# Performance work log

Hardware: AMD Instinct MI355X
Metric: run time of the kernel (lower is better)

The kernel has to match this reference:

```python
import jax, jax.numpy as jnp
import numpy as np

V = 32000
MASK_ID = 31999
EPS = 1e-3          # log-linear schedule eps
DT = 0.05           # reverse-step size
NUCLEUS_P = 0.9
NEG_INF = -1000000.0
B, S = 2, 1024


def move_chance(t):
    # BD3-LM log-linear schedule: move_chance(t) = (1 - eps) * t
    return (1.0 - EPS) * t


def nucleus_filter(probs, p):
    # descending sort over vocab
    order = jnp.argsort(-probs, axis=-1)                     # [B,S,V]
    sorted_probs = jnp.take_along_axis(probs, order, axis=-1)
    cum = jnp.cumsum(sorted_probs, axis=-1)
    keep = cum <= p
    keep = keep.at[..., 0].set(True)                          # always keep top-1
    kept = sorted_probs * keep
    inv = jnp.argsort(order, axis=-1)                         # inverse permutation
    filtered = jnp.take_along_axis(kept, inv, axis=-1)        # scatter back
    return filtered / jnp.sum(filtered, axis=-1, keepdims=True)


def setup_inputs() -> dict:
    key = jax.random.key(0)
    k1, k2, k3, k4 = jax.random.split(key, 4)
    x = jax.random.randint(k1, (B, S), 0, V, dtype=jnp.int32)
    m = jax.random.uniform(k4, (B, S)) < 0.5
    x = jnp.where(m, MASK_ID, x)
    logits = jax.random.normal(k2, (B, S, V), dtype=jnp.float32)
    t = jnp.ones((1,), dtype=jnp.float32)
    u = jax.random.uniform(k3, (B, S, V), dtype=jnp.float32)
    return {"x": x, "logits": logits, "t": t, "u": u}


def reference(x, logits, t, u):
    mct = move_chance(t)[..., None]          # [1,1]
    mcs = move_chance(t - DT)[..., None]     # [1,1]
    mask_prob = mcs / mct                    # [1,1], broadcasts over [S,V]

    logits = logits.at[:, :, MASK_ID].set(NEG_INF)
    p_x0 = jax.nn.softmax(logits, axis=-1)   # [B,S,V]
    p_x0 = nucleus_filter(p_x0, NUCLEUS_P)

    q_xs = p_x0 * (1.0 - mask_prob)
    q_xs = q_xs.at[:, :, MASK_ID].set(jnp.squeeze(mask_prob, -1))

    gumbel = -jnp.log(-jnp.log(u + 1e-10) + 1e-10)
    x_new = jnp.argmax(q_xs / (gumbel + 1e-10), axis=-1).astype(x.dtype)

    is_masked = x == MASK_ID
    x_new = jnp.where(is_masked, x_new, x)
    return x_new, p_x0
```

## Files before the change

kernel.cpp:

```cpp
#include <hip/hip_runtime.h>

#define NVOC 32000
#define NV4  (NVOC / 4)
#define MASKID 31999
#define NBINS 1024
#define NTHR 1024
#define LISTCAP 2048

typedef unsigned int u32;
typedef unsigned long long u64;

__device__ __forceinline__ int bin_e(float e) {
    int v = (int)(__float_as_uint(e) >> 17) - 6976;
    v = v < 0 ? 0 : v;
    return v > (NBINS - 1) ? (NBINS - 1) : v;
}

__device__ __forceinline__ u32 fix32(float e) {
    float x = e * 4294967296.0f;
    x = fminf(x, 4294967040.0f);
    return (u32)x;
}

__device__ __forceinline__ u64 shfl_down_u64(u64 v, int off) {
    u32 lo = (u32)(v & 0xFFFFFFFFULL);
    u32 hi = (u32)(v >> 32);
    lo = __shfl_down(lo, off, 64);
    hi = __shfl_down(hi, off, 64);
    return (((u64)hi) << 32) | lo;
}

__global__ __launch_bounds__(NTHR, 8) void mdlm_kernel(
    const int* __restrict__ xin,
    const float* __restrict__ logits,
    const float* __restrict__ tin,
    const float* __restrict__ uin,
    float* __restrict__ out,
    int rows)
{
    __shared__ u64 sHist[NBINS];
    __shared__ u32 sList[LISTCAP];
    __shared__ double sRedD[16];
    __shared__ float sRedF[16];
    __shared__ int sRedI[16];
    __shared__ u64 sRedU[16];
    __shared__ float sZmax, sTT;
    __shared__ int sCnt, sB, sCross, sMaxDrop;
    __shared__ u32 sTau;
    __shared__ u64 sZ, sAs, sSfp;

    const int row = blockIdx.x;
    if (row >= rows) return;
    const int tid = threadIdx.x;
    const float4* lrow4 = (const float4*)(logits + (size_t)row * NVOC);
    const float* urow = uin + (size_t)row * NVOC;
    float* prow = out + (size_t)rows + (size_t)row * NVOC;

    sHist[tid] = 0ULL;
    if (tid == 0) {
        sCnt = 0; sB = -1; sCross = 0; sMaxDrop = -1; sTau = 0xFFFFFFFFu;
        sZ = 0ULL; sSfp = 0ULL; sAs = 0ULL;
        sTT = tin[0];
    }
    __syncthreads();

    float lmax = -3.0e38f;
    for (int v4 = tid; v4 < NV4; v4 += NTHR) {
        float4 f = lrow4[v4];
        if (v4 == (MASKID >> 2)) f.w = -1000000.0f;
        lmax = fmaxf(lmax, fmaxf(fmaxf(f.x, f.y), fmaxf(f.z, f.w)));
    }
    for (int off = 32; off > 0; off >>= 1)
        lmax = fmaxf(lmax, __shfl_down(lmax, off, 64));
    if ((tid & 63) == 0) sRedF[tid >> 6] = lmax;
    __syncthreads();
    if (tid == 0) {
        float m = sRedF[0];
        for (int w = 1; w < NTHR / 64; ++w) m = fmaxf(m, sRedF[w]);
        sZmax = m;
    }
    __syncthreads();
    const float zmax = sZmax;

    u64 zloc = 0ULL;
    for (int v4 = tid; v4 < NV4; v4 += NTHR) {
        float4 f = lrow4[v4];
        if (v4 == (MASKID >> 2)) f.w = -1000000.0f;
        float zz[4] = {f.x, f.y, f.z, f.w};
#pragma unroll
        for (int e4 = 0; e4 < 4; ++e4) {
            float e = __expf(zz[e4] - zmax);
            u32 m = fix32(e);
            atomicAdd(&sHist[bin_e(e)], (u64)m);
            zloc += m;
        }
    }
    for (int off = 32; off > 0; off >>= 1) zloc += shfl_down_u64(zloc, off);
    if ((tid & 63) == 0) sRedU[tid >> 6] = zloc;
    __syncthreads();
    if (tid == 0) {
        u64 z = 0ULL;
        for (int w = 0; w < NTHR / 64; ++w) z += sRedU[w];
        sZ = z;
    }
    __syncthreads();
    const double T = 0.9 * (double)sZ;

    for (int dlt = 1; dlt < NBINS; dlt <<= 1) {
        u64 vv = (tid + dlt < NBINS) ? sHist[tid + dlt] : 0ULL;
        __syncthreads();
        sHist[tid] += vv;
        __syncthreads();
    }
    {
        u64 Ai = sHist[tid];
        u64 As = (tid + 1 < NBINS) ? sHist[tid + 1] : 0ULL;
        bool dropped = ((double)As >= T);
        bool keptf = ((double)Ai <= T);
        if (dropped) atomicMax(&sMaxDrop, tid);
        if (!dropped && !keptf) { sB = tid; sCross = 1; }
    }
    __syncthreads();
    if (tid == 0) {
        int B = sCross ? sB : sMaxDrop;
        sB = B;
        u64 As;
        if (B < 0) As = sHist[0];
        else As = (B + 1 < NBINS) ? sHist[B + 1] : 0ULL;
        sAs = As;
        if (!sCross) sSfp = As;
    }
    __syncthreads();

    const int Bst = sB;
    const int cross = sCross;

    if (cross) {
        for (int v4 = tid; v4 < NV4; v4 += NTHR) {
            float4 f = lrow4[v4];
            if (v4 == (MASKID >> 2)) f.w = -1000000.0f;
            float zz[4] = {f.x, f.y, f.z, f.w};
#pragma unroll
            for (int e4 = 0; e4 < 4; ++e4) {
                float e = __expf(zz[e4] - zmax);
                if (bin_e(e) == Bst) {
                    u32 m = fix32(e);
                    int pos = atomicAdd(&sCnt, 1);
                    if (pos < LISTCAP) sList[pos] = m;
                }
            }
        }
        __syncthreads();
        const int K = sCnt < LISTCAP ? sCnt : LISTCAP;
        for (int jj = tid; jj < K; jj += NTHR) {
            u32 mj = sList[jj];
            u64 s = sAs;
            for (int q2 = 0; q2 < K; ++q2) {
                u32 mv = sList[q2];
                if (mv >= mj) s += (u64)mv;
            }
            if ((double)s <= T) atomicMin(&sTau, mj);
        }
        __syncthreads();
        if (tid == 0) sSfp = sAs;
        __syncthreads();
        u32 tl = sTau;
        if (tl != 0xFFFFFFFFu) {
            u64 part = 0ULL;
            for (int q2 = tid; q2 < K; q2 += NTHR) {
                u32 mv = sList[q2];
                if (mv >= tl) part += (u64)mv;
            }
            if (part) atomicAdd(&sSfp, part);
        }
        __syncthreads();
    }

    u32 tauU;
    {
        u32 tv = sTau;
        u32 edgefix = 0u;
        if (Bst >= 0) edgefix = fix32(__uint_as_float((u32)(Bst + 1 + 6976) << 17));
        if (cross) tauU = (tv != 0xFFFFFFFFu) ? tv : edgefix;
        else       tauU = (Bst < 0) ? 0u : edgefix;
    }

    const double invSd = 4294967296.0 / (double)sSfp;
    const float invSf = (float)invSd;

    const double td = (double)sTT;
    const double mpd = ((1.0 - 1e-3) * (td - 0.05)) / ((1.0 - 1e-3) * td);
    const double omd = 1.0 - mpd;
    const float mpf = (float)mpd;
    const float omf = (float)omd;

    float r1 = -3.0e38f, r2 = -3.0e38f;
    int   i1 = 0,        i2 = 0;
    float e1 = 0.0f,     e2 = 0.0f;
    float u1 = 0.0f,     u2 = 0.0f;
    for (int v4 = tid; v4 < NV4; v4 += NTHR) {
        float4 uf = ((const float4*)urow)[v4];
        float4 f = lrow4[v4];
        if (v4 == (MASKID >> 2)) f.w = -1000000.0f;
        float uu[4] = {uf.x, uf.y, uf.z, uf.w};
        float zz[4] = {f.x, f.y, f.z, f.w};
        float pp[4];
        const int i0 = v4 * 4;
#pragma unroll
        for (int e4 = 0; e4 < 4; ++e4) {
            const int i = i0 + e4;
            float e = __expf(zz[e4] - zmax);
            bool kept = (fix32(e) >= tauU);
            float p = kept ? e * invSf : 0.0f;
            pp[e4] = p;
            float q = p * omf;
            float ug = uu[e4] + 1e-10f;
            float l1 = __logf(ug);
            float w = 1e-10f - l1;
            float g = -__logf(w);
            float r = q * __builtin_amdgcn_rcpf(g + 1e-10f);
            if (r > r1) {
                r2 = r1; i2 = i1; e2 = e1; u2 = u1;
                r1 = r;  i1 = i;  e1 = e;  u1 = uu[e4];
            } else if (r > r2) {
                r2 = r;  i2 = i;  e2 = e;  u2 = uu[e4];
            }
        }
        float4 po;
        po.x = pp[0]; po.y = pp[1]; po.z = pp[2]; po.w = pp[3];
        ((float4*)prow)[v4] = po;
    }
    if (tid == ((MASKID >> 2) & (NTHR - 1))) {
        float um = urow[MASKID];
        float ug = um + 1e-10f;
        float l1 = __logf(ug);
        float w = 1e-10f - l1;
        float g = -__logf(w);
        float rm = mpf * __builtin_amdgcn_rcpf(g + 1e-10f);
        if (rm > r1) {
            r2 = r1; i2 = i1; e2 = e1; u2 = u1;
            r1 = rm; i1 = MASKID; e1 = 0.0f; u1 = um;
        } else if (rm > r2) {
            r2 = rm; i2 = MASKID; e2 = 0.0f; u2 = um;
        }
    }

    double best; int bidx;
    {
        double q;
        if (i1 == MASKID) q = mpd;
        else {
            bool k = (fix32(e1) >= tauU);
            q = k ? (double)e1 * invSd * omd : 0.0;
        }
        double g = -log(-log((double)u1 + 1e-10) + 1e-10);
        best = q / (g + 1e-10);
        bidx = i1;
    }
    {
        double q;
        if (i2 == MASKID) q = mpd;
        else {
            bool k = (fix32(e2) >= tauU);
            q = k ? (double)e2 * invSd * omd : 0.0;
        }
        double g = -log(-log((double)u2 + 1e-10) + 1e-10);
        double rd = q / (g + 1e-10);
        if (rd > best || (rd == best && i2 < bidx)) { best = rd; bidx = i2; }
    }

    for (int off = 32; off > 0; off >>= 1) {
        double ov = __shfl_down(best, off, 64);
        int oi = __shfl_down(bidx, off, 64);
        if (ov > best || (ov == best && oi < bidx)) { best = ov; bidx = oi; }
    }
    if ((tid & 63) == 0) { sRedD[tid >> 6] = best; sRedI[tid >> 6] = bidx; }
    __syncthreads();
    if (tid == 0) {
        best = sRedD[0]; bidx = sRedI[0];
        for (int w = 1; w < NTHR / 64; ++w) {
            double ov = sRedD[w]; int oi = sRedI[w];
            if (ov > best || (ov == best && oi < bidx)) { best = ov; bidx = oi; }
        }
        int xv = xin[row];
        out[row] = (float)((xv == MASKID) ? bidx : xv);
    }
}

extern "C" void kernel_launch(void* const* d_in, const int* in_sizes, int n_in,
                              void* d_out, int out_size, void* d_ws, size_t ws_size,
                              hipStream_t stream) {
    const int* x = (const int*)d_in[0];
    const float* logits = (const float*)d_in[1];
    const float* t = (const float*)d_in[2];
    const float* u = (const float*)d_in[3];
    float* out = (float*)d_out;
    const int rows = in_sizes[0];
    hipLaunchKernelGGL(mdlm_kernel, dim3(rows), dim3(NTHR), 0, stream,
                       x, logits, t, u, out, rows);
}
```

Before: 265.2 us.

## Keep exp'd logits in registers across passes instead of reloading and recomputing

Loads each row's logits once into a per-thread register array (8 float4 per thread), computes exp once, and reuses those values in the histogram, crossing-bin list, and final sampling passes. This removes two extra global reads of the logits row and the repeated exp. The total mass is now taken from the suffix-scanned histogram instead of a separate u64 reduction. The cost is higher register pressure at 1024 threads per block, which could cause spills or lower occupancy.

```diff
diff --git a/kernel.cpp b/kernel.cpp
--- a/kernel.cpp
+++ b/kernel.cpp
@@ -6,6 +6,7 @@
 #define NBINS 1024
 #define NTHR 1024
 #define LISTCAP 2048
+#define KITER 8
 
 typedef unsigned int u32;
 typedef unsigned long long u64;
@@ -20,14 +21,6 @@
     float x = e * 4294967296.0f;
     x = fminf(x, 4294967040.0f);
     return (u32)x;
-}
-
-__device__ __forceinline__ u64 shfl_down_u64(u64 v, int off) {
-    u32 lo = (u32)(v & 0xFFFFFFFFULL);
-    u32 hi = (u32)(v >> 32);
-    lo = __shfl_down(lo, off, 64);
-    hi = __shfl_down(hi, off, 64);
-    return (((u64)hi) << 32) | lo;
 }
 
 __global__ __launch_bounds__(NTHR, 8) void mdlm_kernel(
@@ -43,32 +36,39 @@
     __shared__ double sRedD[16];
     __shared__ float sRedF[16];
     __shared__ int sRedI[16];
-    __shared__ u64 sRedU[16];
     __shared__ float sZmax, sTT;
     __shared__ int sCnt, sB, sCross, sMaxDrop;
     __shared__ u32 sTau;
-    __shared__ u64 sZ, sAs, sSfp;
+    __shared__ u64 sAs, sSfp;
 
     const int row = blockIdx.x;
     if (row >= rows) return;
     const int tid = threadIdx.x;
     const float4* lrow4 = (const float4*)(logits + (size_t)row * NVOC);
-    const float* urow = uin + (size_t)row * NVOC;
+    const float4* urow4 = (const float4*)(uin + (size_t)row * NVOC);
     float* prow = out + (size_t)rows + (size_t)row * NVOC;
 
     sHist[tid] = 0ULL;
     if (tid == 0) {
         sCnt = 0; sB = -1; sCross = 0; sMaxDrop = -1; sTau = 0xFFFFFFFFu;
-        sZ = 0ULL; sSfp = 0ULL; sAs = 0ULL;
+        sAs = 0ULL; sSfp = 0ULL;
         sTT = tin[0];
     }
     __syncthreads();
 
+    float4 ez[KITER];
     float lmax = -3.0e38f;
-    for (int v4 = tid; v4 < NV4; v4 += NTHR) {
-        float4 f = lrow4[v4];
-        if (v4 == (MASKID >> 2)) f.w = -1000000.0f;
-        lmax = fmaxf(lmax, fmaxf(fmaxf(f.x, f.y), fmaxf(f.z, f.w)));
+#pragma unroll
+    for (int k = 0; k < KITER; ++k) {
+        const int v4 = tid + k * NTHR;
+        if (v4 < NV4) {
+            float4 f = lrow4[v4];
+            if (v4 == (MASKID >> 2)) f.w = -1000000.0f;
+            ez[k] = f;
+            lmax = fmaxf(lmax, fmaxf(fmaxf(f.x, f.y), fmaxf(f.z, f.w)));
+        } else {
+            ez[k] = make_float4(-1.0e38f, -1.0e38f, -1.0e38f, -1.0e38f);
+        }
     }
     for (int off = 32; off > 0; off >>= 1)
         lmax = fmaxf(lmax, __shfl_down(lmax, off, 64));
@@ -82,29 +82,23 @@
     __syncthreads();
     const float zmax = sZmax;
 
-    u64 zloc = 0ULL;
-    for (int v4 = tid; v4 < NV4; v4 += NTHR) {
-        float4 f = lrow4[v4];
-        if (v4 == (MASKID >> 2)) f.w = -1000000.0f;
-        float zz[4] = {f.x, f.y, f.z, f.w};
-#pragma unroll
-        for (int e4 = 0; e4 < 4; ++e4) {
-            float e = __expf(zz[e4] - zmax);
-            u32 m = fix32(e);
-            atomicAdd(&sHist[bin_e(e)], (u64)m);
-            zloc += m;
-        }
-    }
-    for (int off = 32; off > 0; off >>= 1) zloc += shfl_down_u64(zloc, off);
-    if ((tid & 63) == 0) sRedU[tid >> 6] = zloc;
-    __syncthreads();
-    if (tid == 0) {
-        u64 z = 0ULL;
-        for (int w = 0; w < NTHR / 64; ++w) z += sRedU[w];
-        sZ = z;
-    }
-    __syncthreads();
-    const double T = 0.9 * (double)sZ;
+#pragma unroll
+    for (int k = 0; k < KITER; ++k) {
+        const int v4 = tid + k * NTHR;
+        float4 f = ez[k];
+        f.x = __expf(f.x - zmax);
+        f.y = __expf(f.y - zmax);
+        f.z = __expf(f.z - zmax);
+        f.w = __expf(f.w - zmax);
+        ez[k] = f;
+        if (v4 < NV4) {
+            atomicAdd(&sHist[bin_e(f.x)], (u64)fix32(f.x));
+            atomicAdd(&sHist[bin_e(f.y)], (u64)fix32(f.y));
+            atomicAdd(&sHist[bin_e(f.z)], (u64)fix32(f.z));
+            atomicAdd(&sHist[bin_e(f.w)], (u64)fix32(f.w));
+        }
+    }
+    __syncthreads();
 
     for (int dlt = 1; dlt < NBINS; dlt <<= 1) {
         u64 vv = (tid + dlt < NBINS) ? sHist[tid + dlt] : 0ULL;
@@ -112,6 +106,7 @@
         sHist[tid] += vv;
         __syncthreads();
     }
+    const double T = 0.9 * (double)sHist[0];
     {
         u64 Ai = sHist[tid];
         u64 As = (tid + 1 < NBINS) ? sHist[tid + 1] : 0ULL;
@@ -136,17 +131,18 @@
     const int cross = sCross;
 
     if (cross) {
-        for (int v4 = tid; v4 < NV4; v4 += NTHR) {
-            float4 f = lrow4[v4];
-            if (v4 == (MASKID >> 2)) f.w = -1000000.0f;
-            float zz[4] = {f.x, f.y, f.z, f.w};
-#pragma unroll
-            for (int e4 = 0; e4 < 4; ++e4) {
-                float e = __expf(zz[e4] - zmax);
-                if (bin_e(e) == Bst) {
-                    u32 m = fix32(e);
-                    int pos = atomicAdd(&sCnt, 1);
-                    if (pos < LISTCAP) sList[pos] = m;
+#pragma unroll
+        for (int k = 0; k < KITER; ++k) {
+            const int v4 = tid + k * NTHR;
+            if (v4 < NV4) {
+                float4 f = ez[k];
+                float ee[4] = {f.x, f.y, f.z, f.w};
+#pragma unroll
+                for (int e4 = 0; e4 < 4; ++e4) {
+                    if (bin_e(ee[e4]) == Bst) {
+                        int pos = atomicAdd(&sCnt, 1);
+                        if (pos < LISTCAP) sList[pos] = fix32(ee[e4]);
+                    }
                 }
             }
         }
@@ -198,40 +194,43 @@
     int   i1 = 0,        i2 = 0;
     float e1 = 0.0f,     e2 = 0.0f;
     float u1 = 0.0f,     u2 = 0.0f;
-    for (int v4 = tid; v4 < NV4; v4 += NTHR) {
-        float4 uf = ((const float4*)urow)[v4];
-        float4 f = lrow4[v4];
-        if (v4 == (MASKID >> 2)) f.w = -1000000.0f;
-        float uu[4] = {uf.x, uf.y, uf.z, uf.w};
-        float zz[4] = {f.x, f.y, f.z, f.w};
-        float pp[4];
-        const int i0 = v4 * 4;
-#pragma unroll
-        for (int e4 = 0; e4 < 4; ++e4) {
-            const int i = i0 + e4;
-            float e = __expf(zz[e4] - zmax);
-            bool kept = (fix32(e) >= tauU);
-            float p = kept ? e * invSf : 0.0f;
-            pp[e4] = p;
-            float q = p * omf;
-            float ug = uu[e4] + 1e-10f;
-            float l1 = __logf(ug);
-            float w = 1e-10f - l1;
-            float g = -__logf(w);
-            float r = q * __builtin_amdgcn_rcpf(g + 1e-10f);
-            if (r > r1) {
-                r2 = r1; i2 = i1; e2 = e1; u2 = u1;
-                r1 = r;  i1 = i;  e1 = e;  u1 = uu[e4];
-            } else if (r > r2) {
-                r2 = r;  i2 = i;  e2 = e;  u2 = uu[e4];
+#pragma unroll
+    for (int k = 0; k < KITER; ++k) {
+        const int v4 = tid + k * NTHR;
+        if (v4 < NV4) {
+            float4 uf = urow4[v4];
+            float4 f = ez[k];
+            float uu[4] = {uf.x, uf.y, uf.z, uf.w};
+            float ee[4] = {f.x, f.y, f.z, f.w};
+            float pp[4];
+            const int i0 = v4 * 4;
+#pragma unroll
+            for (int e4 = 0; e4 < 4; ++e4) {
+                const int i = i0 + e4;
+                float e = ee[e4];
+                bool kept = (fix32(e) >= tauU);
+                float p = kept ? e * invSf : 0.0f;
+                pp[e4] = p;
+                float q = p * omf;
+                float ug = uu[e4] + 1e-10f;
+                float l1 = __logf(ug);
+                float w = 1e-10f - l1;
+                float g = -__logf(w);
+                float r = q * __builtin_amdgcn_rcpf(g + 1e-10f);
+                if (r > r1) {
+                    r2 = r1; i2 = i1; e2 = e1; u2 = u1;
+                    r1 = r;  i1 = i;  e1 = e;  u1 = uu[e4];
+                } else if (r > r2) {
+                    r2 = r;  i2 = i;  e2 = e;  u2 = uu[e4];
+                }
             }
-        }
-        float4 po;
-        po.x = pp[0]; po.y = pp[1]; po.z = pp[2]; po.w = pp[3];
-        ((float4*)prow)[v4] = po;
+            float4 po;
+            po.x = pp[0]; po.y = pp[1]; po.z = pp[2]; po.w = pp[3];
+            ((float4*)prow)[v4] = po;
+        }
     }
     if (tid == ((MASKID >> 2) & (NTHR - 1))) {
-        float um = urow[MASKID];
+        float um = ((const float*)urow4)[MASKID];
         float ug = um + 1e-10f;
         float l1 = __logf(ug);
         float w = 1e-10f - l1;
@@ -269,17 +268,19 @@
         if (rd > best || (rd == best && i2 < bidx)) { best = rd; bidx = i2; }
     }
 
+    const int NW = NTHR / 64;
+    __shared__ double sBestD[NTHR / 64];
     for (int off = 32; off > 0; off >>= 1) {
         double ov = __shfl_down(best, off, 64);
         int oi = __shfl_down(bidx, off, 64);
         if (ov > best || (ov == best && oi < bidx)) { best = ov; bidx = oi; }
     }
-    if ((tid & 63) == 0) { sRedD[tid >> 6] = best; sRedI[tid >> 6] = bidx; }
+    if ((tid & 63) == 0) { sBestD[tid >> 6] = best; sRedI[tid >> 6] = bidx; }
     __syncthreads();
     if (tid == 0) {
-        best = sRedD[0]; bidx = sRedI[0];
-        for (int w = 1; w < NTHR / 64; ++w) {
-            double ov = sRedD[w]; int oi = sRedI[w];
+        best = sBestD[0]; bidx = sRedI[0];
+        for (int w = 1; w < NW; ++w) {
+            double ov = sBestD[w]; int oi = sRedI[w];
             if (ov > best || (ov == best && oi < bidx)) { best = ov; bidx = oi; }
         }
         int xv = xin[row];
```

Result: slower. 389.4 us (+46.9%).
